# Kernel optimization log

Hardware: AMD Instinct MI355X
Metric: run time of the kernel (lower is better)

The kernel has to match this reference:

```python
import jax, jax.numpy as jnp
import numpy as np

EMBED = 1024
HEAD = 64
SEQ = 2048
BATCH = 8


def setup_inputs() -> dict:
    key = jax.random.key(0)
    kx, kq, kk, kv = jax.random.split(key, 4)
    x = jax.random.normal(kx, (BATCH, SEQ, EMBED), dtype=jnp.float32)
    # torch nn.Linear weight is [out,in]; we store [in,out] so y = x @ W
    Wq = jax.random.normal(kq, (EMBED, HEAD), dtype=jnp.float32) * (EMBED ** -0.5)
    Wk = jax.random.normal(kk, (EMBED, HEAD), dtype=jnp.float32) * (EMBED ** -0.5)
    Wv = jax.random.normal(kv, (EMBED, HEAD), dtype=jnp.float32) * (EMBED ** -0.5)
    return {"x": x, "Wq": Wq, "Wk": Wk, "Wv": Wv}


def reference(x, Wq, Wk, Wv):
    # x: [B,T,C]; single-head causal attention. Scale uses C (embedding dim),
    # matching the original module's C ** (-0.5). Dropout in eval mode (identity).
    B, T, C = x.shape
    q = x @ Wq  # [B,T,H]
    k = x @ Wk  # [B,T,H]
    v = x @ Wv  # [B,T,H]
    scores = jnp.einsum('bqh,bkh->bqk', q, k) * (C ** -0.5)  # [B,T,T]
    causal = jnp.tril(jnp.ones((T, T), dtype=bool))
    scores = jnp.where(causal, scores, -jnp.inf)
    weights = jax.nn.softmax(scores, axis=-1)
    return jnp.einsum('bqk,bkh->bqh', weights, v)  # [B,T,H]
```

## Files before the change

### kernel.cpp

```cpp
#include <hip/hip_runtime.h>
#include <hip/hip_bf16.h>
#include <math.h>

#define BATCH 8
#define SEQ 2048
#define EMBED 1024
#define HEAD 64
#define NROWS (BATCH*SEQ)

typedef short bf16x8 __attribute__((ext_vector_type(8)));
typedef short bf16x4 __attribute__((ext_vector_type(4)));
typedef float f32x4  __attribute__((ext_vector_type(4)));

__device__ inline short f2bf(float f) {
    __hip_bfloat16 h = __float2bfloat16(f);
    return *(short*)&h;
}
__device__ inline float bf2f(short s) {
    __hip_bfloat16 h = *(__hip_bfloat16*)&s;
    return __bfloat162float(h);
}

#define NSLOT128 72
__device__ inline int triOff128(int t) {
    int g = t >> 1, r = t & 1;
    return (g + r) * (g + 1);
}

__global__ __launch_bounds__(256) void prep_w(
    const float* __restrict__ Wq, const float* __restrict__ Wk,
    const float* __restrict__ Wv, short* __restrict__ wt)
{
    int g    = blockIdx.x * 256 + threadIdx.x;
    int lane = g & 63;
    int frag = g >> 6;
    int k32  = frag & 31;
    int ct   = frag >> 5;
    int col  = ct * 16 + (lane & 15);
    int mm   = col >> 6, cc = col & 63;
    const float* W = (mm == 0) ? Wq : ((mm == 1) ? Wk : Wv);
    int kb = k32 * 32 + (lane >> 4) * 8;
    bf16x8 o;
#pragma unroll
    for (int j = 0; j < 8; j++)
        o[j] = f2bf(W[(size_t)(kb + j) * HEAD + cc]);
    *(bf16x8*)&wt[(size_t)g * 8] = o;
}

__global__ __launch_bounds__(512, 4) void proj_kernel(
    const float* __restrict__ x, const short* __restrict__ wt,
    short* __restrict__ q, short* __restrict__ k, short* __restrict__ vt)
{
    __shared__ short xs[32][1024];
    float* psum = (float*)&xs[0][0];

    const int tid  = threadIdx.x;
    const int wave = tid >> 6, lane = tid & 63;
    const int m16  = lane & 15, quad = lane >> 4;
    const int cg   = wave & 3;
    const int kh   = wave >> 2;
    const int r0   = blockIdx.x * 32;

    {
        const int row  = tid >> 4;
        const int col4 = tid & 15;
        const float* xr = x + (size_t)(r0 + row) * EMBED;
#pragma unroll
        for (int h = 0; h < 2; h++) {
            float4 f[8];
#pragma unroll
            for (int i = 0; i < 8; i++)
                f[i] = *(const float4*)&xr[(h * 8 + i) * 64 + col4 * 4];
#pragma unroll
            for (int i = 0; i < 8; i++) {
                int c  = (h * 8 + i) * 64 + col4 * 4;
                int k8 = c >> 3, rem = c & 7;
                int cs = ((k8 ^ (row & 7)) << 3) + rem;
                bf16x4 bv;
                bv[0] = f2bf(f[i].x); bv[1] = f2bf(f[i].y);
                bv[2] = f2bf(f[i].z); bv[3] = f2bf(f[i].w);
                *(bf16x4*)&xs[row][cs] = bv;
            }
        }
    }
    __syncthreads();

    f32x4 acc[2][3];
#pragma unroll
    for (int mt = 0; mt < 2; mt++)
#pragma unroll
        for (int j = 0; j < 3; j++) acc[mt][j] = (f32x4){0.f, 0.f, 0.f, 0.f};

#pragma unroll 4
    for (int s = 0; s < 16; s++) {
        int k32  = kh * 16 + s;
        int ksw  = ((k32 * 4 + quad) ^ (m16 & 7)) << 3;
        bf16x8 a0 = *(const bf16x8*)&xs[m16][ksw];
        bf16x8 a1 = *(const bf16x8*)&xs[16 + m16][ksw];
#pragma unroll
        for (int j = 0; j < 3; j++) {
            int ct = cg * 3 + j;
            bf16x8 bb = *(const bf16x8*)&wt[(size_t)((ct * 32 + k32) * 64 + lane) * 8];
            acc[0][j] = __builtin_amdgcn_mfma_f32_16x16x32_bf16(a0, bb, acc[0][j], 0, 0, 0);
            acc[1][j] = __builtin_amdgcn_mfma_f32_16x16x32_bf16(a1, bb, acc[1][j], 0, 0, 0);
        }
    }

    __syncthreads();
    if (kh == 1) {
        float* p = psum + ((size_t)(cg * 64 + lane) * 24);
#pragma unroll
        for (int mt = 0; mt < 2; mt++)
#pragma unroll
            for (int j = 0; j < 3; j++)
                *(f32x4*)&p[(mt * 3 + j) * 4] = acc[mt][j];
    }
    __syncthreads();
    if (kh == 0) {
        const float* p = psum + ((size_t)(cg * 64 + lane) * 24);
        const int bb = r0 >> 11;
        const int tb = r0 & 2047;
#pragma unroll
        for (int mt = 0; mt < 2; mt++)
#pragma unroll
            for (int j = 0; j < 3; j++) {
                f32x4 o = acc[mt][j] + *(const f32x4*)&p[(mt * 3 + j) * 4];
                int gcol = (cg * 3 + j) * 16 + m16;
                int mm = gcol >> 6, cc = gcol & 63;
                if (mm < 2) {
                    short* op = (mm == 0) ? q : k;
#pragma unroll
                    for (int reg = 0; reg < 4; reg++) {
                        int row = r0 + mt * 16 + quad * 4 + reg;
                        op[(size_t)row * HEAD + cc] = f2bf(o[reg]);
                    }
                } else {
                    bf16x4 pk;
                    pk[0] = f2bf(o[0]); pk[1] = f2bf(o[1]);
                    pk[2] = f2bf(o[2]); pk[3] = f2bf(o[3]);
                    int t = tb + mt * 16 + quad * 4;
                    *(bf16x4*)&vt[(((size_t)bb * 64 + cc) << 11) + t] = pk;
                }
            }
    }
}

__global__ __launch_bounds__(512, 4) void attn_kernel(
    const short* __restrict__ qg, const short* __restrict__ kg,
    const short* __restrict__ vtg,
    short* __restrict__ pO, float* __restrict__ pl)
{
    __shared__ short ksh[64][72];
    __shared__ short vsh[64][72];
    __shared__ short psh[8][16][72];

    const int t   = blockIdx.x;
    const int seg = blockIdx.y;
    const int b   = blockIdx.z;
    const int c0  = seg * 4;
    const int c1  = min(c0 + 4, 2 * t + 2);
    if (c0 >= c1) return;

    const int tid  = threadIdx.x;
    const int wave = tid >> 6, lane = tid & 63;
    const int m16  = lane & 15, quad = lane >> 4;
    const int qtile = t * 8 + wave;
    const int own   = qtile >> 2;
    const float scale = 0.03125f;

    const short* qb  = qg  + (size_t)b * SEQ * HEAD;
    const short* kb  = kg  + (size_t)b * SEQ * HEAD;
    const short* vtb = vtg + (size_t)b * HEAD * SEQ;

    bf16x8 a_q0, a_q1;
    {
        const int qrow = qtile * 16 + m16;
        a_q0 = *(const bf16x8*)&qb[(size_t)qrow * HEAD + quad * 8];
        a_q1 = *(const bf16x8*)&qb[(size_t)qrow * HEAD + 32 + quad * 8];
    }

    f32x4 o_acc[4];
#pragma unroll
    for (int i = 0; i < 4; i++) o_acc[i] = (f32x4){0.f, 0.f, 0.f, 0.f};
    float lsum[4] = {0.f, 0.f, 0.f, 0.f};

    const int srow = tid >> 3;
    const int sc8  = (tid & 7) * 8;

    bf16x8 kr = *(const bf16x8*)&kb[(size_t)(c0 * 64 + srow) * HEAD + sc8];
    bf16x8 vr = *(const bf16x8*)&vtb[((size_t)srow << 11) + c0 * 64 + sc8];

    for (int c = c0; c < c1; c++) {
        const int t0 = c * 64;
        __syncthreads();
        *(bf16x8*)&ksh[srow][sc8] = kr;
        *(bf16x8*)&vsh[srow][sc8] = vr;
        __syncthreads();
        if (c + 1 < c1) {
            const int tn = (c + 1) * 64;
            kr = *(const bf16x8*)&kb[(size_t)(tn + srow) * HEAD + sc8];
            vr = *(const bf16x8*)&vtb[((size_t)srow << 11) + tn + sc8];
        }
        if (c > own) continue;

        f32x4 s_t[4];
#pragma unroll
        for (int nt = 0; nt < 4; nt++) {
            bf16x8 bk0 = *(const bf16x8*)&ksh[nt * 16 + m16][quad * 8];
            bf16x8 bk1 = *(const bf16x8*)&ksh[nt * 16 + m16][32 + quad * 8];
            f32x4 acc = (f32x4){0.f, 0.f, 0.f, 0.f};
            acc = __builtin_amdgcn_mfma_f32_16x16x32_bf16(a_q0, bk0, acc, 0, 0, 0);
            acc = __builtin_amdgcn_mfma_f32_16x16x32_bf16(a_q1, bk1, acc, 0, 0, 0);
            s_t[nt] = acc;
        }

        if (c == own) {
#pragma unroll
            for (int r = 0; r < 4; r++) {
                const int row = qtile * 16 + quad * 4 + r;
#pragma unroll
                for (int nt = 0; nt < 4; nt++) {
                    int tt = t0 + nt * 16 + m16;
                    float p = (tt <= row) ? __expf(s_t[nt][r] * scale) : 0.f;
                    lsum[r] += p;
                    psh[wave][quad * 4 + r][nt * 16 + m16] = f2bf(p);
                }
            }
        } else {
#pragma unroll
            for (int r = 0; r < 4; r++) {
#pragma unroll
                for (int nt = 0; nt < 4; nt++) {
                    float p = __expf(s_t[nt][r] * scale);
                    lsum[r] += p;
                    psh[wave][quad * 4 + r][nt * 16 + m16] = f2bf(p);
                }
            }
        }

#pragma unroll
        for (int s = 0; s < 2; s++) {
            bf16x8 a_p = *(const bf16x8*)&psh[wave][m16][s * 32 + quad * 8];
#pragma unroll
            for (int ht = 0; ht < 4; ht++) {
                bf16x8 b_v = *(const bf16x8*)&vsh[ht * 16 + m16][s * 32 + quad * 8];
                o_acc[ht] = __builtin_amdgcn_mfma_f32_16x16x32_bf16(a_p, b_v, o_acc[ht], 0, 0, 0);
            }
        }
    }

#pragma unroll
    for (int r = 0; r < 4; r++) {
#pragma unroll
        for (int off = 8; off >= 1; off >>= 1)
            lsum[r] += __shfl_xor(lsum[r], off, 64);
    }
    const size_t slot  = (size_t)b * NSLOT128 + triOff128(t) + seg;
    const size_t pbase = slot * 128;
#pragma unroll
    for (int ht = 0; ht < 4; ht++) {
#pragma unroll
        for (int r = 0; r < 4; r++) {
            int rowt = wave * 16 + quad * 4 + r;
            pO[(pbase + rowt) * 64 + ht * 16 + m16] = f2bf(o_acc[ht][r]);
        }
    }
    if (m16 == 0) {
#pragma unroll
        for (int r = 0; r < 4; r++) {
            int rowt = wave * 16 + quad * 4 + r;
            pl[pbase + rowt] = lsum[r];
        }
    }
}

__global__ __launch_bounds__(256) void combine_kernel(
    const short* __restrict__ pO, const float* __restrict__ pl,
    float* __restrict__ out)
{
    int g    = blockIdx.x * 256 + threadIdx.x;
    int h4   = (g & 15) * 4;
    int row  = (g >> 4) & 2047;
    int b    = g >> 15;
    int t    = row >> 7, rowt = row & 127;
    int ns   = (t >> 1) + 1;
    size_t base = (size_t)b * NSLOT128 + triOff128(t);
    float4 O = {0.f, 0.f, 0.f, 0.f};
    float  L = 0.f;
    for (int s = 0; s < ns; s++) {
        bf16x4 ov = *(const bf16x4*)&pO[((base + s) * 128 + rowt) * 64 + h4];
        O.x += bf2f(ov[0]); O.y += bf2f(ov[1]);
        O.z += bf2f(ov[2]); O.w += bf2f(ov[3]);
        L += pl[(base + s) * 128 + rowt];
    }
    float inv = 1.f / L;
    O.x *= inv; O.y *= inv; O.z *= inv; O.w *= inv;
    *(float4*)&out[(size_t)g * 4] = O;
}

extern "C" void kernel_launch(void* const* d_in, const int* in_sizes, int n_in,
                              void* d_out, int out_size, void* d_ws, size_t ws_size,
                              hipStream_t stream) {
    const float* x  = (const float*)d_in[0];
    const float* Wq = (const float*)d_in[1];
    const float* Wk = (const float*)d_in[2];
    const float* Wv = (const float*)d_in[3];
    float* out = (float*)d_out;

    short* q  = (short*)d_ws;
    short* k  = q + (size_t)NROWS * HEAD;
    short* vt = k + (size_t)NROWS * HEAD;
    short* wt = vt + (size_t)NROWS * HEAD;
    short* pO = wt + 196608;
    float* pl = (float*)(pO + (size_t)BATCH * NSLOT128 * 128 * 64);

    prep_w<<<96, 256, 0, stream>>>(Wq, Wk, Wv, wt);
    proj_kernel<<<512, 512, 0, stream>>>(x, wt, q, k, vt);
    attn_kernel<<<dim3(16, 8, 8), 512, 0, stream>>>(q, k, vt, pO, pl);
    combine_kernel<<<1024, 256, 0, stream>>>(pO, pl, out);
}
```

Baseline: 129.6 us.

## Fuse split-K combine into attention via last-block atomic counter and compact grid

Removes the separate combine kernel. Each attention block increments a per-(batch, query-tile) counter, and the last segment to finish reads the other segments' partial outputs and sums from global memory and writes the normalized result. The grid is also compacted from a padded 3D grid with early-exit blocks to a dense 1D triangular slot index, decoded with a small loop. In exchange it adds a threadfence, an atomic and a serial tail of work in the last block, and it depends on the counters being zeroed in prep_w.

```diff
diff --git a/kernel.cpp b/kernel.cpp
--- a/kernel.cpp
+++ b/kernel.cpp
@@ -29,9 +29,10 @@
 
 __global__ __launch_bounds__(256) void prep_w(
     const float* __restrict__ Wq, const float* __restrict__ Wk,
-    const float* __restrict__ Wv, short* __restrict__ wt)
+    const float* __restrict__ Wv, short* __restrict__ wt, int* __restrict__ cnt)
 {
     int g    = blockIdx.x * 256 + threadIdx.x;
+    if (g < BATCH * 16) cnt[g] = 0;
     int lane = g & 63;
     int frag = g >> 6;
     int k32  = frag & 31;
@@ -148,18 +149,22 @@
 __global__ __launch_bounds__(512, 4) void attn_kernel(
     const short* __restrict__ qg, const short* __restrict__ kg,
     const short* __restrict__ vtg,
-    short* __restrict__ pO, float* __restrict__ pl)
+    short* __restrict__ pO, float* __restrict__ pl,
+    int* __restrict__ cnt, float* __restrict__ out)
 {
     __shared__ short ksh[64][72];
     __shared__ short vsh[64][72];
     __shared__ short psh[8][16][72];
-
-    const int t   = blockIdx.x;
-    const int seg = blockIdx.y;
-    const int b   = blockIdx.z;
+    __shared__ int isLast;
+
+    const int s = blockIdx.x;
+    const int b = blockIdx.y;
+    int t = 0;
+    while (t < 15 && s >= triOff128(t + 1)) t++;
+    const int seg = s - triOff128(t);
+    const int ns  = (t >> 1) + 1;
     const int c0  = seg * 4;
     const int c1  = min(c0 + 4, 2 * t + 2);
-    if (c0 >= c1) return;
 
     const int tid  = threadIdx.x;
     const int wave = tid >> 6, lane = tid & 63;
@@ -239,11 +244,11 @@
         }
 
 #pragma unroll
-        for (int s = 0; s < 2; s++) {
-            bf16x8 a_p = *(const bf16x8*)&psh[wave][m16][s * 32 + quad * 8];
+        for (int ss = 0; ss < 2; ss++) {
+            bf16x8 a_p = *(const bf16x8*)&psh[wave][m16][ss * 32 + quad * 8];
 #pragma unroll
             for (int ht = 0; ht < 4; ht++) {
-                bf16x8 b_v = *(const bf16x8*)&vsh[ht * 16 + m16][s * 32 + quad * 8];
+                bf16x8 b_v = *(const bf16x8*)&vsh[ht * 16 + m16][ss * 32 + quad * 8];
                 o_acc[ht] = __builtin_amdgcn_mfma_f32_16x16x32_bf16(a_p, b_v, o_acc[ht], 0, 0, 0);
             }
         }
@@ -255,8 +260,9 @@
         for (int off = 8; off >= 1; off >>= 1)
             lsum[r] += __shfl_xor(lsum[r], off, 64);
     }
-    const size_t slot  = (size_t)b * NSLOT128 + triOff128(t) + seg;
-    const size_t pbase = slot * 128;
+
+    const size_t base  = (size_t)b * NSLOT128 + triOff128(t);
+    const size_t pbase = ((size_t)b * NSLOT128 + s) * 128;
 #pragma unroll
     for (int ht = 0; ht < 4; ht++) {
 #pragma unroll
@@ -272,30 +278,36 @@
             pl[pbase + rowt] = lsum[r];
         }
     }
-}
-
-__global__ __launch_bounds__(256) void combine_kernel(
-    const short* __restrict__ pO, const float* __restrict__ pl,
-    float* __restrict__ out)
-{
-    int g    = blockIdx.x * 256 + threadIdx.x;
-    int h4   = (g & 15) * 4;
-    int row  = (g >> 4) & 2047;
-    int b    = g >> 15;
-    int t    = row >> 7, rowt = row & 127;
-    int ns   = (t >> 1) + 1;
-    size_t base = (size_t)b * NSLOT128 + triOff128(t);
-    float4 O = {0.f, 0.f, 0.f, 0.f};
-    float  L = 0.f;
-    for (int s = 0; s < ns; s++) {
-        bf16x4 ov = *(const bf16x4*)&pO[((base + s) * 128 + rowt) * 64 + h4];
-        O.x += bf2f(ov[0]); O.y += bf2f(ov[1]);
-        O.z += bf2f(ov[2]); O.w += bf2f(ov[3]);
-        L += pl[(base + s) * 128 + rowt];
-    }
-    float inv = 1.f / L;
-    O.x *= inv; O.y *= inv; O.z *= inv; O.w *= inv;
-    *(float4*)&out[(size_t)g * 4] = O;
+
+    __threadfence();
+    __syncthreads();
+    if (tid == 0) {
+        int old = atomicAdd(&cnt[b * 16 + t], 1);
+        isLast = (old == ns - 1);
+    }
+    __syncthreads();
+    if (!isLast) return;
+    __threadfence();
+
+#pragma unroll
+    for (int r = 0; r < 4; r++) {
+        const int rowt = wave * 16 + quad * 4 + r;
+        float L = lsum[r];
+        for (int s2 = 0; s2 < ns; s2++) {
+            if (s2 == seg) continue;
+            L += pl[(base + s2) * 128 + rowt];
+        }
+        const float invL = 1.f / L;
+#pragma unroll
+        for (int ht = 0; ht < 4; ht++) {
+            float O = o_acc[ht][r];
+            for (int s2 = 0; s2 < ns; s2++) {
+                if (s2 == seg) continue;
+                O += bf2f(pO[((base + s2) * 128 + rowt) * 64 + ht * 16 + m16]);
+            }
+            out[(((size_t)b * SEQ) + t * 128 + rowt) * HEAD + ht * 16 + m16] = O * invL;
+        }
+    }
 }
 
 extern "C" void kernel_launch(void* const* d_in, const int* in_sizes, int n_in,
@@ -313,9 +325,9 @@
     short* wt = vt + (size_t)NROWS * HEAD;
     short* pO = wt + 196608;
     float* pl = (float*)(pO + (size_t)BATCH * NSLOT128 * 128 * 64);
-
-    prep_w<<<96, 256, 0, stream>>>(Wq, Wk, Wv, wt);
+    int*  cnt = (int*)(pl + (size_t)BATCH * NSLOT128 * 128);
+
+    prep_w<<<96, 256, 0, stream>>>(Wq, Wk, Wv, wt, cnt);
     proj_kernel<<<512, 512, 0, stream>>>(x, wt, q, k, vt);
-    attn_kernel<<<dim3(16, 8, 8), 512, 0, stream>>>(q, k, vt, pO, pl);
-    combine_kernel<<<1024, 256, 0, stream>>>(pO, pl, out);
-}
+    attn_kernel<<<dim3(NSLOT128, BATCH), 512, 0, stream>>>(q, k, vt, pO, pl, cnt, out);
+}
```

Result: slower. 335.9 us (+159.2%).

## Shrink attention query tile to 64 rows and preload all KV chunks once

Applied to the files above, without the earlier changes.

The attention kernel now uses 256-thread blocks covering 64 query rows instead of 512-thread blocks covering 128. Each block loads its full segment of four K/V chunks into shared memory up front with a single barrier, replacing the per-chunk double-barrier staging loop. Smaller tiles remove the waves that sat idle on chunks beyond their causal range. The cost is more partial-result slots for the combine kernel and a larger shared-memory footprint per block, with no overlap between loading and compute.

```diff
diff --git a/kernel.cpp b/kernel.cpp
--- a/kernel.cpp
+++ b/kernel.cpp
@@ -21,10 +21,10 @@
     return __bfloat162float(h);
 }
 
-#define NSLOT128 72
-__device__ inline int triOff128(int t) {
-    int g = t >> 1, r = t & 1;
-    return (g + r) * (g + 1);
+#define NSLOT 144
+__device__ __host__ inline int triOff(int qt) {
+    int g = qt >> 2;
+    return 2 * g * (g + 1) + (qt & 3) * (g + 1);
 }
 
 __global__ __launch_bounds__(256) void prep_w(
@@ -145,27 +145,26 @@
     }
 }
 
-__global__ __launch_bounds__(512, 4) void attn_kernel(
+__global__ __launch_bounds__(256, 2) void attn_kernel(
     const short* __restrict__ qg, const short* __restrict__ kg,
     const short* __restrict__ vtg,
     short* __restrict__ pO, float* __restrict__ pl)
 {
-    __shared__ short ksh[64][72];
-    __shared__ short vsh[64][72];
-    __shared__ short psh[8][16][72];
-
-    const int t   = blockIdx.x;
+    __shared__ short ksh[256][72];
+    __shared__ short vsh[64][264];
+    __shared__ short psh[4][16][72];
+
+    const int qt  = blockIdx.x;
     const int seg = blockIdx.y;
     const int b   = blockIdx.z;
     const int c0  = seg * 4;
-    const int c1  = min(c0 + 4, 2 * t + 2);
+    const int c1  = min(c0 + 4, qt + 1);
     if (c0 >= c1) return;
+    const int nch = c1 - c0;
 
     const int tid  = threadIdx.x;
     const int wave = tid >> 6, lane = tid & 63;
     const int m16  = lane & 15, quad = lane >> 4;
-    const int qtile = t * 8 + wave;
-    const int own   = qtile >> 2;
     const float scale = 0.03125f;
 
     const short* qb  = qg  + (size_t)b * SEQ * HEAD;
@@ -174,50 +173,53 @@
 
     bf16x8 a_q0, a_q1;
     {
-        const int qrow = qtile * 16 + m16;
+        const int qrow = qt * 64 + wave * 16 + m16;
         a_q0 = *(const bf16x8*)&qb[(size_t)qrow * HEAD + quad * 8];
         a_q1 = *(const bf16x8*)&qb[(size_t)qrow * HEAD + 32 + quad * 8];
     }
 
+    {
+        const int kt  = tid >> 2;
+        const int kh8 = (tid & 3) * 16;
+#pragma unroll
+        for (int cc = 0; cc < 4; cc++) {
+            const int t0 = (c0 + cc) * 64;
+            bf16x8 k0 = *(const bf16x8*)&kb[(size_t)(t0 + kt) * HEAD + kh8];
+            bf16x8 k1 = *(const bf16x8*)&kb[(size_t)(t0 + kt) * HEAD + kh8 + 8];
+            *(bf16x8*)&ksh[cc * 64 + kt][kh8]     = k0;
+            *(bf16x8*)&ksh[cc * 64 + kt][kh8 + 8] = k1;
+            bf16x8 v0 = *(const bf16x8*)&vtb[((size_t)kt << 11) + t0 + kh8];
+            bf16x8 v1 = *(const bf16x8*)&vtb[((size_t)kt << 11) + t0 + kh8 + 8];
+            *(bf16x8*)&vsh[kt][cc * 64 + kh8]     = v0;
+            *(bf16x8*)&vsh[kt][cc * 64 + kh8 + 8] = v1;
+        }
+    }
+    __syncthreads();
+
     f32x4 o_acc[4];
 #pragma unroll
     for (int i = 0; i < 4; i++) o_acc[i] = (f32x4){0.f, 0.f, 0.f, 0.f};
     float lsum[4] = {0.f, 0.f, 0.f, 0.f};
 
-    const int srow = tid >> 3;
-    const int sc8  = (tid & 7) * 8;
-
-    bf16x8 kr = *(const bf16x8*)&kb[(size_t)(c0 * 64 + srow) * HEAD + sc8];
-    bf16x8 vr = *(const bf16x8*)&vtb[((size_t)srow << 11) + c0 * 64 + sc8];
-
-    for (int c = c0; c < c1; c++) {
+    for (int cc = 0; cc < nch; cc++) {
+        const int c  = c0 + cc;
         const int t0 = c * 64;
-        __syncthreads();
-        *(bf16x8*)&ksh[srow][sc8] = kr;
-        *(bf16x8*)&vsh[srow][sc8] = vr;
-        __syncthreads();
-        if (c + 1 < c1) {
-            const int tn = (c + 1) * 64;
-            kr = *(const bf16x8*)&kb[(size_t)(tn + srow) * HEAD + sc8];
-            vr = *(const bf16x8*)&vtb[((size_t)srow << 11) + tn + sc8];
-        }
-        if (c > own) continue;
 
         f32x4 s_t[4];
 #pragma unroll
         for (int nt = 0; nt < 4; nt++) {
-            bf16x8 bk0 = *(const bf16x8*)&ksh[nt * 16 + m16][quad * 8];
-            bf16x8 bk1 = *(const bf16x8*)&ksh[nt * 16 + m16][32 + quad * 8];
+            bf16x8 bk0 = *(const bf16x8*)&ksh[cc * 64 + nt * 16 + m16][quad * 8];
+            bf16x8 bk1 = *(const bf16x8*)&ksh[cc * 64 + nt * 16 + m16][32 + quad * 8];
             f32x4 acc = (f32x4){0.f, 0.f, 0.f, 0.f};
             acc = __builtin_amdgcn_mfma_f32_16x16x32_bf16(a_q0, bk0, acc, 0, 0, 0);
             acc = __builtin_amdgcn_mfma_f32_16x16x32_bf16(a_q1, bk1, acc, 0, 0, 0);
             s_t[nt] = acc;
         }
 
-        if (c == own) {
+        if (c == qt) {
 #pragma unroll
             for (int r = 0; r < 4; r++) {
-                const int row = qtile * 16 + quad * 4 + r;
+                const int row = qt * 64 + wave * 16 + quad * 4 + r;
 #pragma unroll
                 for (int nt = 0; nt < 4; nt++) {
                     int tt = t0 + nt * 16 + m16;
@@ -239,11 +241,11 @@
         }
 
 #pragma unroll
-        for (int s = 0; s < 2; s++) {
-            bf16x8 a_p = *(const bf16x8*)&psh[wave][m16][s * 32 + quad * 8];
+        for (int ss = 0; ss < 2; ss++) {
+            bf16x8 a_p = *(const bf16x8*)&psh[wave][m16][ss * 32 + quad * 8];
 #pragma unroll
             for (int ht = 0; ht < 4; ht++) {
-                bf16x8 b_v = *(const bf16x8*)&vsh[ht * 16 + m16][s * 32 + quad * 8];
+                bf16x8 b_v = *(const bf16x8*)&vsh[ht * 16 + m16][cc * 64 + ss * 32 + quad * 8];
                 o_acc[ht] = __builtin_amdgcn_mfma_f32_16x16x32_bf16(a_p, b_v, o_acc[ht], 0, 0, 0);
             }
         }
@@ -255,8 +257,8 @@
         for (int off = 8; off >= 1; off >>= 1)
             lsum[r] += __shfl_xor(lsum[r], off, 64);
     }
-    const size_t slot  = (size_t)b * NSLOT128 + triOff128(t) + seg;
-    const size_t pbase = slot * 128;
+    const size_t slot  = (size_t)b * NSLOT + triOff(qt) + seg;
+    const size_t pbase = slot * 64;
 #pragma unroll
     for (int ht = 0; ht < 4; ht++) {
 #pragma unroll
@@ -278,20 +280,20 @@
     const short* __restrict__ pO, const float* __restrict__ pl,
     float* __restrict__ out)
 {
-    int g    = blockIdx.x * 256 + threadIdx.x;
-    int h4   = (g & 15) * 4;
-    int row  = (g >> 4) & 2047;
-    int b    = g >> 15;
-    int t    = row >> 7, rowt = row & 127;
-    int ns   = (t >> 1) + 1;
-    size_t base = (size_t)b * NSLOT128 + triOff128(t);
+    int g   = blockIdx.x * 256 + threadIdx.x;
+    int h4  = (g & 15) * 4;
+    int row = (g >> 4) & 2047;
+    int b   = g >> 15;
+    int qt  = row >> 6, lr = row & 63;
+    int ns  = (qt >> 2) + 1;
+    size_t base = (size_t)b * NSLOT + triOff(qt);
     float4 O = {0.f, 0.f, 0.f, 0.f};
     float  L = 0.f;
     for (int s = 0; s < ns; s++) {
-        bf16x4 ov = *(const bf16x4*)&pO[((base + s) * 128 + rowt) * 64 + h4];
+        bf16x4 ov = *(const bf16x4*)&pO[((base + s) * 64 + lr) * 64 + h4];
         O.x += bf2f(ov[0]); O.y += bf2f(ov[1]);
         O.z += bf2f(ov[2]); O.w += bf2f(ov[3]);
-        L += pl[(base + s) * 128 + rowt];
+        L += pl[(base + s) * 64 + lr];
     }
     float inv = 1.f / L;
     O.x *= inv; O.y *= inv; O.z *= inv; O.w *= inv;
@@ -312,10 +314,10 @@
     short* vt = k + (size_t)NROWS * HEAD;
     short* wt = vt + (size_t)NROWS * HEAD;
     short* pO = wt + 196608;
-    float* pl = (float*)(pO + (size_t)BATCH * NSLOT128 * 128 * 64);
+    float* pl = (float*)(pO + (size_t)BATCH * NSLOT * 64 * 64);
 
     prep_w<<<96, 256, 0, stream>>>(Wq, Wk, Wv, wt);
     proj_kernel<<<512, 512, 0, stream>>>(x, wt, q, k, vt);
-    attn_kernel<<<dim3(16, 8, 8), 512, 0, stream>>>(q, k, vt, pO, pl);
+    attn_kernel<<<dim3(32, 8, 8), 256, 0, stream>>>(q, k, vt, pO, pl);
     combine_kernel<<<1024, 256, 0, stream>>>(pO, pl, out);
 }
```

Result: slower. 133.2 us (+2.8%).
